# Optimization experiments

Measured on AMD Instinct MI355X. Metric: run time of the kernel, lower is better.

The kernel has to match this reference:

```python
import jax, jax.numpy as jnp
import numpy as np

T, B, F_IN, H, N_CLS = 1000, 256, 13, 100, 20


def setup_inputs() -> dict:
    key = jax.random.key(0)
    ks = jax.random.split(key, 10)
    s_in = 1.0 / np.sqrt(H)
    inp = {
        "mfcc0": jax.random.normal(ks[0], (T, B, F_IN), jnp.float32),
        "mfcc1": jax.random.normal(ks[1], (T, B, F_IN), jnp.float32),
        "mfcc2": jax.random.normal(ks[2], (T, B, F_IN), jnp.float32),
        "len0": jnp.full((B,), float(T), jnp.float32),
        # GRU params (PyTorch layout: gates [r, z, n] stacked -> 3H rows)
        "W_ih": jax.random.uniform(ks[3], (3 * H, 3 * F_IN), jnp.float32, -s_in, s_in),
        "W_hh": jax.random.uniform(ks[4], (3 * H, H), jnp.float32, -s_in, s_in),
        "b_ih": jax.random.uniform(ks[5], (3 * H,), jnp.float32, -s_in, s_in),
        "b_hh": jax.random.uniform(ks[6], (3 * H,), jnp.float32, -s_in, s_in),
        # output linear: Linear(200, 20)
        "W_out": jax.random.uniform(ks[7], (N_CLS, 2 * H), jnp.float32, -1/np.sqrt(2*H), 1/np.sqrt(2*H)),
        "b_out": jax.random.uniform(ks[8], (N_CLS,), jnp.float32, -1/np.sqrt(2*H), 1/np.sqrt(2*H)),
    }
    return inp


def _gru(x, W_ih, W_hh, b_ih, b_hh):
    # x: [T, B, 39] -> enc_out: [T, B, H]
    gi = jnp.einsum('tbi,gi->tbg', x, W_ih) + b_ih  # precompute input gates [T,B,3H]

    def step(h, gi_t):
        gh = h @ W_hh.T + b_hh                       # [B,3H]
        i_r, i_z, i_n = jnp.split(gi_t, 3, axis=-1)
        h_r, h_z, h_n = jnp.split(gh, 3, axis=-1)
        r = jax.nn.sigmoid(i_r + h_r)
        z = jax.nn.sigmoid(i_z + h_z)
        n = jnp.tanh(i_n + r * h_n)
        h_new = (1.0 - z) * n + z * h
        return h_new, h_new

    h0 = jnp.zeros((x.shape[1], W_hh.shape[1]), x.dtype)
    _, enc_out = jax.lax.scan(step, h0, gi)
    return enc_out


def reference(mfcc0, mfcc1, mfcc2, len0, W_ih, W_hh, b_ih, b_hh, W_out, b_out):
    x = jnp.concatenate([mfcc0, mfcc1, mfcc2], axis=2)   # [T,B,39]
    enc_out = _gru(x, W_ih, W_hh, b_ih, b_hh)             # [T,B,H]
    avg_pool = enc_out.sum(0) / len0[:, None]             # [B,H]
    max_pool = enc_out.max(0)                             # [B,H]
    feat = jnp.concatenate([avg_pool, max_pool], axis=1)  # [B,2H]
    return feat @ W_out.T + b_out                         # [B,20]
```

## Files before the change

kernel.cpp:

```cpp
#include <hip/hip_runtime.h>
#include <math.h>

#define T_STEPS 1000
#define BATCH   256
#define FIN     13
#define XDIM    39
#define XPAD    40
#define HDIM    100
#define G3      300
#define NCLS    20

__launch_bounds__(320, 1)
__global__ void gru_persistent(const float* __restrict__ mfcc0,
                               const float* __restrict__ mfcc1,
                               const float* __restrict__ mfcc2,
                               const float* __restrict__ len0,
                               const float* __restrict__ W_ih,
                               const float* __restrict__ W_hh,
                               const float* __restrict__ b_ih,
                               const float* __restrict__ b_hh,
                               const float* __restrict__ W_out,
                               const float* __restrict__ b_out,
                               float* __restrict__ out)
{
    const int b   = blockIdx.x;
    const int tid = threadIdx.x;

    __shared__ float h_lds[2][HDIM];
    __shared__ float x_lds[2][XPAD];
    __shared__ float gates[G3];
    __shared__ float ghn[HDIM];
    __shared__ float feat[2*HDIM];

    float wih[XPAD];
    float whh[HDIM];
    float bi = 0.f, bh = 0.f;
    if (tid < G3) {
        #pragma unroll
        for (int i = 0; i < XDIM; ++i) wih[i] = W_ih[tid * XDIM + i];
        wih[XDIM] = 0.f;
        #pragma unroll
        for (int k = 0; k < HDIM; ++k) whh[k] = W_hh[tid * HDIM + k];
        bi = b_ih[tid];
        bh = b_hh[tid];
    }

    const float* xsrc = mfcc0;
    int xoff = 0;
    if (tid < XDIM) {
        const int f = tid % FIN;
        xsrc = (tid < FIN) ? mfcc0 : (tid < 2 * FIN ? mfcc1 : mfcc2);
        xoff = b * FIN + f;
    }

    if (tid < HDIM) h_lds[0][tid] = 0.f;
    if (tid < XDIM) x_lds[0][tid] = xsrc[xoff];
    if (tid == XDIM) { x_lds[0][XDIM] = 0.f; x_lds[1][XDIM] = 0.f; }
    __syncthreads();

    float sum = 0.f;
    float mx  = -INFINITY;

    for (int t = 0; t < T_STEPS; ++t) {
        const int cur = t & 1;
        const int nxt = cur ^ 1;

        float xpf = 0.f;
        if (tid < XDIM && (t + 1) < T_STEPS)
            xpf = xsrc[(size_t)(t + 1) * (BATCH * FIN) + xoff];

        if (tid < G3) {
            float ai = bi;
            float ah = bh;
            const float4* x4 = (const float4*)x_lds[cur];
            #pragma unroll
            for (int i = 0; i < XPAD / 4; ++i) {
                const float4 v = x4[i];
                ai = fmaf(wih[4*i+0], v.x, ai);
                ai = fmaf(wih[4*i+1], v.y, ai);
                ai = fmaf(wih[4*i+2], v.z, ai);
                ai = fmaf(wih[4*i+3], v.w, ai);
            }
            const float4* h4 = (const float4*)h_lds[cur];
            #pragma unroll
            for (int k = 0; k < HDIM / 4; ++k) {
                const float4 v = h4[k];
                ah = fmaf(whh[4*k+0], v.x, ah);
                ah = fmaf(whh[4*k+1], v.y, ah);
                ah = fmaf(whh[4*k+2], v.z, ah);
                ah = fmaf(whh[4*k+3], v.w, ah);
            }
            if (tid < 2 * HDIM) {
                gates[tid] = ai + ah;
            } else {
                gates[tid]      = ai;
                ghn[tid - 2*HDIM] = ah;
            }
        }
        if (tid < XDIM) x_lds[nxt][tid] = xpf;
        __syncthreads();

        if (tid < HDIM) {
            const float r  = 1.f / (1.f + expf(-gates[tid]));
            const float z  = 1.f / (1.f + expf(-gates[HDIM + tid]));
            const float n  = tanhf(fmaf(r, ghn[tid], gates[2*HDIM + tid]));
            const float ho = h_lds[cur][tid];
            const float hv = fmaf(z, ho - n, n);
            h_lds[nxt][tid] = hv;
            sum += hv;
            mx = fmaxf(mx, hv);
        }
        __syncthreads();
    }

    if (tid < HDIM) {
        feat[tid]        = sum / len0[b];
        feat[HDIM + tid] = mx;
    }
    __syncthreads();

    if (tid < NCLS) {
        float acc = b_out[tid];
        #pragma unroll 4
        for (int k = 0; k < 2 * HDIM; ++k)
            acc = fmaf(W_out[tid * 2 * HDIM + k], feat[k], acc);
        out[b * NCLS + tid] = acc;
    }
}

extern "C" void kernel_launch(void* const* d_in, const int* in_sizes, int n_in,
                              void* d_out, int out_size, void* d_ws, size_t ws_size,
                              hipStream_t stream)
{
    const float* mfcc0 = (const float*)d_in[0];
    const float* mfcc1 = (const float*)d_in[1];
    const float* mfcc2 = (const float*)d_in[2];
    const float* len0  = (const float*)d_in[3];
    const float* W_ih  = (const float*)d_in[4];
    const float* W_hh  = (const float*)d_in[5];
    const float* b_ih  = (const float*)d_in[6];
    const float* b_hh  = (const float*)d_in[7];
    const float* W_out = (const float*)d_in[8];
    const float* b_out = (const float*)d_in[9];
    float* out = (float*)d_out;

    gru_persistent<<<BATCH, 320, 0, stream>>>(
        mfcc0, mfcc1, mfcc2, len0, W_ih, W_hh, b_ih, b_hh, W_out, b_out, out);
}
```

Measured before the change: 1.161 ms.

## Split recurrent dot products across two thread halves and use fast transcendentals

Doubles the block to 640 threads. The first half computes the input projection plus the first 28 hidden columns, and the second half computes the remaining 72 hidden columns, with partial sums combined in shared memory. Each thread's serial dependency chain per step gets shorter, and four independent accumulators are used. The gate nonlinearities switch to __expf-based sigmoid and tanh, which loses some accuracy, and the larger block plus the occupancy hint of 3 may add register pressure or spilling.

Result: slower. 2.584 ms (+122.7%).

```diff
diff --git a/kernel.cpp b/kernel.cpp
--- a/kernel.cpp
+++ b/kernel.cpp
@@ -9,8 +9,28 @@
 #define HDIM    100
 #define G3      300
 #define NCLS    20
-
-__launch_bounds__(320, 1)
+#define NTHR    640
+#define SPLIT   28
+
+__device__ __forceinline__ float fast_sigmoid(float v) {
+    return 1.f / (1.f + __expf(-v));
+}
+__device__ __forceinline__ float fast_tanh(float v) {
+    const float c = fminf(fmaxf(v, -15.f), 15.f);
+    const float e = __expf(2.f * c);
+    return (e - 1.f) / (e + 1.f);
+}
+
+__device__ __forceinline__ void fma4(const float4& wv, const float4& xv,
+                                     float& a0, float& a1, float& a2, float& a3)
+{
+    a0 = fmaf(wv.x, xv.x, a0);
+    a1 = fmaf(wv.y, xv.y, a1);
+    a2 = fmaf(wv.z, xv.z, a2);
+    a3 = fmaf(wv.w, xv.w, a3);
+}
+
+__launch_bounds__(NTHR, 3)
 __global__ void gru_persistent(const float* __restrict__ mfcc0,
                                const float* __restrict__ mfcc1,
                                const float* __restrict__ mfcc2,
@@ -25,25 +45,38 @@
 {
     const int b   = blockIdx.x;
     const int tid = threadIdx.x;
-
-    __shared__ float h_lds[2][HDIM];
-    __shared__ float x_lds[2][XPAD];
-    __shared__ float gates[G3];
-    __shared__ float ghn[HDIM];
-    __shared__ float feat[2*HDIM];
-
-    float wih[XPAD];
-    float whh[HDIM];
-    float bi = 0.f, bh = 0.f;
-    if (tid < G3) {
-        #pragma unroll
-        for (int i = 0; i < XDIM; ++i) wih[i] = W_ih[tid * XDIM + i];
-        wih[XDIM] = 0.f;
-        #pragma unroll
-        for (int k = 0; k < HDIM; ++k) whh[k] = W_hh[tid * HDIM + k];
-        bi = b_ih[tid];
-        bh = b_hh[tid];
-    }
+    const bool pa = (tid < 320);
+    const int g0  = pa ? tid : (tid - 320);
+    const int g   = (g0 < G3) ? g0 : (G3 - 1);
+
+    __shared__ __align__(16) float h_lds[2][HDIM];
+    __shared__ __align__(16) float x_lds[2][XPAD];
+    __shared__ float p0a[G3];
+    __shared__ float p0h[G3];
+    __shared__ float p1h[G3];
+    __shared__ float feat[2 * HDIM];
+
+    float4 q0, q1, q2, q3, q4, q5, q6, q7, q8, q9, q10, q11, q12, q13, q14, q15, q16, q17;
+    if (pa) {
+        const float* wi = W_ih + g * XDIM;
+#define LDA(i) make_float4(wi[4*(i)], wi[4*(i)+1], wi[4*(i)+2], wi[4*(i)+3])
+        q0 = LDA(0); q1 = LDA(1); q2 = LDA(2); q3 = LDA(3); q4 = LDA(4);
+        q5 = LDA(5); q6 = LDA(6); q7 = LDA(7); q8 = LDA(8);
+        q9 = make_float4(wi[36], wi[37], wi[38], 0.f);
+#undef LDA
+        const float4* wh = (const float4*)(W_hh + g * HDIM);
+        q10 = wh[0]; q11 = wh[1]; q12 = wh[2]; q13 = wh[3];
+        q14 = wh[4]; q15 = wh[5]; q16 = wh[6];
+        q17 = make_float4(0.f, 0.f, 0.f, 0.f);
+    } else {
+        const float4* wh = (const float4*)(W_hh + g * HDIM + SPLIT);
+        q0  = wh[0];  q1  = wh[1];  q2  = wh[2];  q3  = wh[3];  q4  = wh[4];
+        q5  = wh[5];  q6  = wh[6];  q7  = wh[7];  q8  = wh[8];  q9  = wh[9];
+        q10 = wh[10]; q11 = wh[11]; q12 = wh[12]; q13 = wh[13]; q14 = wh[14];
+        q15 = wh[15]; q16 = wh[16]; q17 = wh[17];
+    }
+    const float bi = pa ? b_ih[g] : 0.f;
+    const float bh = pa ? b_hh[g] : 0.f;
 
     const float* xsrc = mfcc0;
     int xoff = 0;
@@ -69,41 +102,67 @@
         if (tid < XDIM && (t + 1) < T_STEPS)
             xpf = xsrc[(size_t)(t + 1) * (BATCH * FIN) + xoff];
 
-        if (tid < G3) {
-            float ai = bi;
-            float ah = bh;
+        if (pa) {
             const float4* x4 = (const float4*)x_lds[cur];
-            #pragma unroll
-            for (int i = 0; i < XPAD / 4; ++i) {
-                const float4 v = x4[i];
-                ai = fmaf(wih[4*i+0], v.x, ai);
-                ai = fmaf(wih[4*i+1], v.y, ai);
-                ai = fmaf(wih[4*i+2], v.z, ai);
-                ai = fmaf(wih[4*i+3], v.w, ai);
+            float i0 = 0.f, i1 = 0.f, i2 = 0.f, i3 = 0.f;
+            float4 vv;
+            vv = x4[0]; fma4(q0, vv, i0, i1, i2, i3);
+            vv = x4[1]; fma4(q1, vv, i0, i1, i2, i3);
+            vv = x4[2]; fma4(q2, vv, i0, i1, i2, i3);
+            vv = x4[3]; fma4(q3, vv, i0, i1, i2, i3);
+            vv = x4[4]; fma4(q4, vv, i0, i1, i2, i3);
+            vv = x4[5]; fma4(q5, vv, i0, i1, i2, i3);
+            vv = x4[6]; fma4(q6, vv, i0, i1, i2, i3);
+            vv = x4[7]; fma4(q7, vv, i0, i1, i2, i3);
+            vv = x4[8]; fma4(q8, vv, i0, i1, i2, i3);
+            vv = x4[9]; fma4(q9, vv, i0, i1, i2, i3);
+
+            const float4* h4 = (const float4*)h_lds[cur];
+            float g0a = 0.f, g1a = 0.f, g2a = 0.f, g3a = 0.f;
+            vv = h4[0]; fma4(q10, vv, g0a, g1a, g2a, g3a);
+            vv = h4[1]; fma4(q11, vv, g0a, g1a, g2a, g3a);
+            vv = h4[2]; fma4(q12, vv, g0a, g1a, g2a, g3a);
+            vv = h4[3]; fma4(q13, vv, g0a, g1a, g2a, g3a);
+            vv = h4[4]; fma4(q14, vv, g0a, g1a, g2a, g3a);
+            vv = h4[5]; fma4(q15, vv, g0a, g1a, g2a, g3a);
+            vv = h4[6]; fma4(q16, vv, g0a, g1a, g2a, g3a);
+            if (g0 < G3) {
+                p0a[g0] = bi + ((i0 + i1) + (i2 + i3));
+                p0h[g0] = bh + ((g0a + g1a) + (g2a + g3a));
             }
-            const float4* h4 = (const float4*)h_lds[cur];
-            #pragma unroll
-            for (int k = 0; k < HDIM / 4; ++k) {
-                const float4 v = h4[k];
-                ah = fmaf(whh[4*k+0], v.x, ah);
-                ah = fmaf(whh[4*k+1], v.y, ah);
-                ah = fmaf(whh[4*k+2], v.z, ah);
-                ah = fmaf(whh[4*k+3], v.w, ah);
-            }
-            if (tid < 2 * HDIM) {
-                gates[tid] = ai + ah;
-            } else {
-                gates[tid]      = ai;
-                ghn[tid - 2*HDIM] = ah;
-            }
+        } else {
+            const float4* h4 = (const float4*)(&h_lds[cur][SPLIT]);
+            float g0a = 0.f, g1a = 0.f, g2a = 0.f, g3a = 0.f;
+            float4 vv;
+            vv = h4[0];  fma4(q0,  vv, g0a, g1a, g2a, g3a);
+            vv = h4[1];  fma4(q1,  vv, g0a, g1a, g2a, g3a);
+            vv = h4[2];  fma4(q2,  vv, g0a, g1a, g2a, g3a);
+            vv = h4[3];  fma4(q3,  vv, g0a, g1a, g2a, g3a);
+            vv = h4[4];  fma4(q4,  vv, g0a, g1a, g2a, g3a);
+            vv = h4[5];  fma4(q5,  vv, g0a, g1a, g2a, g3a);
+            vv = h4[6];  fma4(q6,  vv, g0a, g1a, g2a, g3a);
+            vv = h4[7];  fma4(q7,  vv, g0a, g1a, g2a, g3a);
+            vv = h4[8];  fma4(q8,  vv, g0a, g1a, g2a, g3a);
+            vv = h4[9];  fma4(q9,  vv, g0a, g1a, g2a, g3a);
+            vv = h4[10]; fma4(q10, vv, g0a, g1a, g2a, g3a);
+            vv = h4[11]; fma4(q11, vv, g0a, g1a, g2a, g3a);
+            vv = h4[12]; fma4(q12, vv, g0a, g1a, g2a, g3a);
+            vv = h4[13]; fma4(q13, vv, g0a, g1a, g2a, g3a);
+            vv = h4[14]; fma4(q14, vv, g0a, g1a, g2a, g3a);
+            vv = h4[15]; fma4(q15, vv, g0a, g1a, g2a, g3a);
+            vv = h4[16]; fma4(q16, vv, g0a, g1a, g2a, g3a);
+            vv = h4[17]; fma4(q17, vv, g0a, g1a, g2a, g3a);
+            if (g0 < G3)
+                p1h[g0] = (g0a + g1a) + (g2a + g3a);
         }
         if (tid < XDIM) x_lds[nxt][tid] = xpf;
         __syncthreads();
 
         if (tid < HDIM) {
-            const float r  = 1.f / (1.f + expf(-gates[tid]));
-            const float z  = 1.f / (1.f + expf(-gates[HDIM + tid]));
-            const float n  = tanhf(fmaf(r, ghn[tid], gates[2*HDIM + tid]));
+            const float r  = fast_sigmoid(p0a[tid] + p0h[tid] + p1h[tid]);
+            const float z  = fast_sigmoid(p0a[HDIM + tid] + p0h[HDIM + tid] + p1h[HDIM + tid]);
+            const float hn = p0h[2*HDIM + tid] + p1h[2*HDIM + tid];
+            const float n  = fast_tanh(fmaf(r, hn, p0a[2*HDIM + tid]));
             const float ho = h_lds[cur][tid];
             const float hv = fmaf(z, ho - n, n);
             h_lds[nxt][tid] = hv;
@@ -144,6 +203,6 @@
     const float* b_out = (const float*)d_in[9];
     float* out = (float*)d_out;
 
-    gru_persistent<<<BATCH, 320, 0, stream>>>(
+    gru_persistent<<<BATCH, NTHR, 0, stream>>>(
         mfcc0, mfcc1, mfcc2, len0, W_ih, W_hh, b_ih, b_hh, W_out, b_out, out);
 }
```

## Split GRU gate dot products across three thread groups with packed LDS vector

Applied to the files above, without the earlier changes.

Triples the block to 960 threads so that each gate row's work is split into three partial dot products: the input projection, and the first 52 and last 48 hidden columns. x and h are packed into one shared vector, and partial sums are reduced in the element-wise phase. This shortens the serial FMA chain per step on the recurrent critical path. It also switches to fast __expf-based sigmoid and tanh. The cost is more threads per barrier, extra LDS traffic for partials, and slightly lower transcendental accuracy.

After: 931.1 us. 1.25x faster.

```diff
diff --git a/kernel.cpp b/kernel.cpp
--- a/kernel.cpp
+++ b/kernel.cpp
@@ -5,12 +5,23 @@
 #define BATCH   256
 #define FIN     13
 #define XDIM    39
-#define XPAD    40
 #define HDIM    100
 #define G3      300
 #define NCLS    20
+#define NTHR    960
+#define VLEN    160
+#define CHUNK   52
 
-__launch_bounds__(320, 1)
+__device__ __forceinline__ float fast_sigmoid(float v) {
+    return 1.f / (1.f + __expf(-v));
+}
+__device__ __forceinline__ float fast_tanh(float v) {
+    const float c = fminf(fmaxf(v, -15.f), 15.f);
+    const float e = __expf(2.f * c);
+    return (e - 1.f) / (e + 1.f);
+}
+
+__launch_bounds__(NTHR, 4)
 __global__ void gru_persistent(const float* __restrict__ mfcc0,
                                const float* __restrict__ mfcc1,
                                const float* __restrict__ mfcc2,
@@ -25,25 +36,46 @@
 {
     const int b   = blockIdx.x;
     const int tid = threadIdx.x;
+    const int p   = tid / 320;
+    const int g0  = tid % 320;
+    const int g   = (g0 < G3) ? g0 : (G3 - 1);
 
-    __shared__ float h_lds[2][HDIM];
-    __shared__ float x_lds[2][XPAD];
-    __shared__ float gates[G3];
-    __shared__ float ghn[HDIM];
-    __shared__ float feat[2*HDIM];
+    __shared__ __align__(16) float V[2][VLEN];
+    __shared__ float part[3 * G3];
+    __shared__ float feat[2 * HDIM];
 
-    float wih[XPAD];
-    float whh[HDIM];
-    float bi = 0.f, bh = 0.f;
-    if (tid < G3) {
-        #pragma unroll
-        for (int i = 0; i < XDIM; ++i) wih[i] = W_ih[tid * XDIM + i];
-        wih[XDIM] = 0.f;
-        #pragma unroll
-        for (int k = 0; k < HDIM; ++k) whh[k] = W_hh[tid * HDIM + k];
-        bi = b_ih[tid];
-        bh = b_hh[tid];
-    }
+    const float* src = (p == 0) ? (W_ih + g * XDIM)
+                                : (W_hh + g * HDIM + ((p == 2) ? CHUNK : 0));
+    const int   c    = (p == 0) ? XDIM : ((p == 1) ? CHUNK : (HDIM - CHUNK));
+    const float bias = (p == 0) ? b_ih[g] : ((p == 1) ? b_hh[g] : 0.f);
+    const int   vb0  = (p == 0) ? 0 : ((p == 1) ? 10 : 23);
+
+    float w00 = ( 0 < c) ? src[ 0] : 0.f, w01 = ( 1 < c) ? src[ 1] : 0.f;
+    float w02 = ( 2 < c) ? src[ 2] : 0.f, w03 = ( 3 < c) ? src[ 3] : 0.f;
+    float w04 = ( 4 < c) ? src[ 4] : 0.f, w05 = ( 5 < c) ? src[ 5] : 0.f;
+    float w06 = ( 6 < c) ? src[ 6] : 0.f, w07 = ( 7 < c) ? src[ 7] : 0.f;
+    float w08 = ( 8 < c) ? src[ 8] : 0.f, w09 = ( 9 < c) ? src[ 9] : 0.f;
+    float w10 = (10 < c) ? src[10] : 0.f, w11 = (11 < c) ? src[11] : 0.f;
+    float w12 = (12 < c) ? src[12] : 0.f, w13 = (13 < c) ? src[13] : 0.f;
+    float w14 = (14 < c) ? src[14] : 0.f, w15 = (15 < c) ? src[15] : 0.f;
+    float w16 = (16 < c) ? src[16] : 0.f, w17 = (17 < c) ? src[17] : 0.f;
+    float w18 = (18 < c) ? src[18] : 0.f, w19 = (19 < c) ? src[19] : 0.f;
+    float w20 = (20 < c) ? src[20] : 0.f, w21 = (21 < c) ? src[21] : 0.f;
+    float w22 = (22 < c) ? src[22] : 0.f, w23 = (23 < c) ? src[23] : 0.f;
+    float w24 = (24 < c) ? src[24] : 0.f, w25 = (25 < c) ? src[25] : 0.f;
+    float w26 = (26 < c) ? src[26] : 0.f, w27 = (27 < c) ? src[27] : 0.f;
+    float w28 = (28 < c) ? src[28] : 0.f, w29 = (29 < c) ? src[29] : 0.f;
+    float w30 = (30 < c) ? src[30] : 0.f, w31 = (31 < c) ? src[31] : 0.f;
+    float w32 = (32 < c) ? src[32] : 0.f, w33 = (33 < c) ? src[33] : 0.f;
+    float w34 = (34 < c) ? src[34] : 0.f, w35 = (35 < c) ? src[35] : 0.f;
+    float w36 = (36 < c) ? src[36] : 0.f, w37 = (37 < c) ? src[37] : 0.f;
+    float w38 = (38 < c) ? src[38] : 0.f, w39 = (39 < c) ? src[39] : 0.f;
+    float w40 = (40 < c) ? src[40] : 0.f, w41 = (41 < c) ? src[41] : 0.f;
+    float w42 = (42 < c) ? src[42] : 0.f, w43 = (43 < c) ? src[43] : 0.f;
+    float w44 = (44 < c) ? src[44] : 0.f, w45 = (45 < c) ? src[45] : 0.f;
+    float w46 = (46 < c) ? src[46] : 0.f, w47 = (47 < c) ? src[47] : 0.f;
+    float w48 = (48 < c) ? src[48] : 0.f, w49 = (49 < c) ? src[49] : 0.f;
+    float w50 = (50 < c) ? src[50] : 0.f, w51 = (51 < c) ? src[51] : 0.f;
 
     const float* xsrc = mfcc0;
     int xoff = 0;
@@ -53,9 +85,8 @@
         xoff = b * FIN + f;
     }
 
-    if (tid < HDIM) h_lds[0][tid] = 0.f;
-    if (tid < XDIM) x_lds[0][tid] = xsrc[xoff];
-    if (tid == XDIM) { x_lds[0][XDIM] = 0.f; x_lds[1][XDIM] = 0.f; }
+    if (tid < VLEN) { V[0][tid] = 0.f; V[1][tid] = 0.f; }
+    if (tid < XDIM) V[0][tid] = xsrc[xoff];
     __syncthreads();
 
     float sum = 0.f;
@@ -69,44 +100,36 @@
         if (tid < XDIM && (t + 1) < T_STEPS)
             xpf = xsrc[(size_t)(t + 1) * (BATCH * FIN) + xoff];
 
-        if (tid < G3) {
-            float ai = bi;
-            float ah = bh;
-            const float4* x4 = (const float4*)x_lds[cur];
-            #pragma unroll
-            for (int i = 0; i < XPAD / 4; ++i) {
-                const float4 v = x4[i];
-                ai = fmaf(wih[4*i+0], v.x, ai);
-                ai = fmaf(wih[4*i+1], v.y, ai);
-                ai = fmaf(wih[4*i+2], v.z, ai);
-                ai = fmaf(wih[4*i+3], v.w, ai);
-            }
-            const float4* h4 = (const float4*)h_lds[cur];
-            #pragma unroll
-            for (int k = 0; k < HDIM / 4; ++k) {
-                const float4 v = h4[k];
-                ah = fmaf(whh[4*k+0], v.x, ah);
-                ah = fmaf(whh[4*k+1], v.y, ah);
-                ah = fmaf(whh[4*k+2], v.z, ah);
-                ah = fmaf(whh[4*k+3], v.w, ah);
-            }
-            if (tid < 2 * HDIM) {
-                gates[tid] = ai + ah;
-            } else {
-                gates[tid]      = ai;
-                ghn[tid - 2*HDIM] = ah;
-            }
-        }
-        if (tid < XDIM) x_lds[nxt][tid] = xpf;
+        const float4* V4 = (const float4*)V[cur];
+        float a0 = 0.f, a1 = 0.f, a2 = 0.f, a3 = 0.f;
+        float4 vv;
+        vv = V4[vb0+ 0]; a0=fmaf(w00,vv.x,a0); a1=fmaf(w01,vv.y,a1); a2=fmaf(w02,vv.z,a2); a3=fmaf(w03,vv.w,a3);
+        vv = V4[vb0+ 1]; a0=fmaf(w04,vv.x,a0); a1=fmaf(w05,vv.y,a1); a2=fmaf(w06,vv.z,a2); a3=fmaf(w07,vv.w,a3);
+        vv = V4[vb0+ 2]; a0=fmaf(w08,vv.x,a0); a1=fmaf(w09,vv.y,a1); a2=fmaf(w10,vv.z,a2); a3=fmaf(w11,vv.w,a3);
+        vv = V4[vb0+ 3]; a0=fmaf(w12,vv.x,a0); a1=fmaf(w13,vv.y,a1); a2=fmaf(w14,vv.z,a2); a3=fmaf(w15,vv.w,a3);
+        vv = V4[vb0+ 4]; a0=fmaf(w16,vv.x,a0); a1=fmaf(w17,vv.y,a1); a2=fmaf(w18,vv.z,a2); a3=fmaf(w19,vv.w,a3);
+        vv = V4[vb0+ 5]; a0=fmaf(w20,vv.x,a0); a1=fmaf(w21,vv.y,a1); a2=fmaf(w22,vv.z,a2); a3=fmaf(w23,vv.w,a3);
+        vv = V4[vb0+ 6]; a0=fmaf(w24,vv.x,a0); a1=fmaf(w25,vv.y,a1); a2=fmaf(w26,vv.z,a2); a3=fmaf(w27,vv.w,a3);
+        vv = V4[vb0+ 7]; a0=fmaf(w28,vv.x,a0); a1=fmaf(w29,vv.y,a1); a2=fmaf(w30,vv.z,a2); a3=fmaf(w31,vv.w,a3);
+        vv = V4[vb0+ 8]; a0=fmaf(w32,vv.x,a0); a1=fmaf(w33,vv.y,a1); a2=fmaf(w34,vv.z,a2); a3=fmaf(w35,vv.w,a3);
+        vv = V4[vb0+ 9]; a0=fmaf(w36,vv.x,a0); a1=fmaf(w37,vv.y,a1); a2=fmaf(w38,vv.z,a2); a3=fmaf(w39,vv.w,a3);
+        vv = V4[vb0+10]; a0=fmaf(w40,vv.x,a0); a1=fmaf(w41,vv.y,a1); a2=fmaf(w42,vv.z,a2); a3=fmaf(w43,vv.w,a3);
+        vv = V4[vb0+11]; a0=fmaf(w44,vv.x,a0); a1=fmaf(w45,vv.y,a1); a2=fmaf(w46,vv.z,a2); a3=fmaf(w47,vv.w,a3);
+        vv = V4[vb0+12]; a0=fmaf(w48,vv.x,a0); a1=fmaf(w49,vv.y,a1); a2=fmaf(w50,vv.z,a2); a3=fmaf(w51,vv.w,a3);
+
+        if (g0 < G3)
+            part[p * G3 + g0] = bias + ((a0 + a1) + (a2 + a3));
+        if (tid < XDIM) V[nxt][tid] = xpf;
         __syncthreads();
 
         if (tid < HDIM) {
-            const float r  = 1.f / (1.f + expf(-gates[tid]));
-            const float z  = 1.f / (1.f + expf(-gates[HDIM + tid]));
-            const float n  = tanhf(fmaf(r, ghn[tid], gates[2*HDIM + tid]));
-            const float ho = h_lds[cur][tid];
+            const float r  = fast_sigmoid(part[tid] + part[G3 + tid] + part[2*G3 + tid]);
+            const float z  = fast_sigmoid(part[HDIM + tid] + part[G3 + HDIM + tid] + part[2*G3 + HDIM + tid]);
+            const float hn = part[G3 + 2*HDIM + tid] + part[2*G3 + 2*HDIM + tid];
+            const float n  = fast_tanh(fmaf(r, hn, part[2*HDIM + tid]));
+            const float ho = V[cur][XDIM + 1 + tid];
             const float hv = fmaf(z, ho - n, n);
-            h_lds[nxt][tid] = hv;
+            V[nxt][XDIM + 1 + tid] = hv;
             sum += hv;
             mx = fmaxf(mx, hv);
         }
@@ -144,6 +167,6 @@
     const float* b_out = (const float*)d_in[9];
     float* out = (float*)d_out;
 
-    gru_persistent<<<BATCH, 320, 0, stream>>>(
+    gru_persistent<<<BATCH, NTHR, 0, stream>>>(
         mfcc0, mfcc1, mfcc2, len0, W_ih, W_hh, b_ih, b_hh, W_out, b_out, out);
 }
```
